# Kernel tuning notes

Hardware: AMD Instinct MI355X
Metric: run time of the kernel (lower is better)

The kernel has to match this reference:

```python
import jax, jax.numpy as jnp
import numpy as np

N_NODES = 50000
N_EDGES = 800000
X_DIM, EDGE_DIM, H_DIM, HOUT = 92, 80, 128, 128
N_CONV = 3
N_GRAPHS = 256
BN_EPS = 1e-5


def setup_inputs() -> dict:
    key = jax.random.key(0)
    ks = jax.random.split(key, 16)
    x = jax.random.normal(ks[0], (N_NODES, X_DIM), dtype=jnp.float32)
    edge_index = jax.random.randint(ks[1], (2, N_EDGES), 0, N_NODES, dtype=jnp.int64)
    edge_attr = jax.random.normal(ks[2], (N_EDGES, EDGE_DIM), dtype=jnp.float32)
    batch = jnp.sort(jax.random.randint(ks[3], (N_NODES,), 0, N_GRAPHS, dtype=jnp.int64))
    s = 0.05
    embed_W = jax.random.normal(ks[4], (X_DIM, H_DIM), dtype=jnp.float32) * s
    embed_b = jnp.zeros((H_DIM,), jnp.float32)
    in_dim = 2 * H_DIM + EDGE_DIM
    conv_W = jax.random.normal(ks[5], (N_CONV, in_dim, 2 * H_DIM), dtype=jnp.float32) * s
    conv_b = jnp.zeros((N_CONV, 2 * H_DIM), jnp.float32)
    bn_i_g = jnp.ones((N_CONV, 2 * H_DIM), jnp.float32)
    bn_i_b = jnp.zeros((N_CONV, 2 * H_DIM), jnp.float32)
    bn_o_g = jnp.ones((N_CONV, H_DIM), jnp.float32)
    bn_o_b = jnp.zeros((N_CONV, H_DIM), jnp.float32)
    lin_W = jax.random.normal(ks[6], (H_DIM, HOUT), dtype=jnp.float32) * s
    lin_b = jnp.zeros((HOUT,), jnp.float32)
    out_W = jax.random.normal(ks[7], (HOUT, 1), dtype=jnp.float32) * s
    out_b = jnp.zeros((1,), jnp.float32)
    return {"x": x, "edge_index": edge_index, "edge_attr": edge_attr, "batch": batch,
            "embed_W": embed_W, "embed_b": embed_b, "conv_W": conv_W, "conv_b": conv_b,
            "bn_i_g": bn_i_g, "bn_i_b": bn_i_b, "bn_o_g": bn_o_g, "bn_o_b": bn_o_b,
            "lin_W": lin_W, "lin_b": lin_b, "out_W": out_W, "out_b": out_b}


def _bn(h, gamma, beta):
    # training-mode BatchNorm1d: biased batch statistics
    mu = jnp.mean(h, axis=0)
    var = jnp.mean(jnp.square(h - mu), axis=0)
    return (h - mu) * jax.lax.rsqrt(var + BN_EPS) * gamma + beta


def _cgconv(x, edge_index, edge_attr, W, b, gi, bi, go, bo):
    src, dst = edge_index[0], edge_index[1]
    msg = jnp.concatenate([x[src], edge_attr, x[dst]], axis=1)  # [E, 2h+e]
    msg = msg @ W + b                                           # [E, 2h]
    msg = _bn(msg, gi, bi)
    filt, core = jnp.split(msg, 2, axis=1)
    gated = jax.nn.sigmoid(filt) * jax.nn.softplus(core)        # [E, h]
    agg = jax.ops.segment_sum(gated, src, num_segments=N_NODES)  # [N, h]
    agg = _bn(agg, go, bo)
    return jax.nn.softplus(x + agg)


def reference(x, edge_index, edge_attr, batch, embed_W, embed_b, conv_W, conv_b,
              bn_i_g, bn_i_b, bn_o_g, bn_o_b, lin_W, lin_b, out_W, out_b):
    h = x @ embed_W + embed_b  # [N, h_dim]
    for i in range(N_CONV):
        h = _cgconv(h, edge_index, edge_attr, conv_W[i], conv_b[i],
                    bn_i_g[i], bn_i_b[i], bn_o_g[i], bn_o_b[i])
    # mean pooling per graph
    sums = jax.ops.segment_sum(h, batch, num_segments=N_GRAPHS)
    cnts = jax.ops.segment_sum(jnp.ones((h.shape[0],), h.dtype), batch, num_segments=N_GRAPHS)
    pooled = sums / jnp.maximum(cnts, 1.0)[:, None]  # [G, h_dim]
    g = jax.nn.softplus(pooled @ lin_W + lin_b)
    return g @ out_W + out_b  # [G, 1]
```

## Files before the change

### kernel.cpp

```cpp
#include <hip/hip_runtime.h>

constexpr int NN = 50000;
constexpr int NE = 800000;
constexpr int XD = 92;
constexpr int ED = 80;
constexpr int HD = 128;
constexpr int C2 = 256;
constexpr int IND = 336;
constexpr int NC = 3;
constexpr int NG = 256;
constexpr int NTILES = NE / 64;
constexpr int WSZ_L = 16 * 3 * 64 * 8;
constexpr int WNP_L = 16 * 4 * 64 * 8;

#define DINL __device__ __forceinline__

typedef __attribute__((ext_vector_type(8))) short bf16x8;
typedef __attribute__((ext_vector_type(4))) float f32x4;

DINL short f2bf(float f) {
  unsigned u = __float_as_uint(f);
  u = (u + 0x7fffu + ((u >> 16) & 1u)) >> 16;
  return (short)u;
}
DINL float bf2f(unsigned short u) { return __uint_as_float(((unsigned)u) << 16); }
DINL float rcp_(float x) {
  float r;
  asm("v_rcp_f32 %0, %1" : "=v"(r) : "v"(x));
  return r;
}
DINL float softplusf_(float x) {
  return x > 20.f ? x : log1pf(__expf(x));
}
DINL float gate_(float f, float cr) {
  float e = __expf(-f);
  float s = rcp_(1.f + e);
  float t = __expf(cr);
  float l = (cr > 15.f) ? cr : __logf(1.f + t);
  return s * l;
}

template <int CTRL>
DINL int dpp_i(int old_, int src) {
  return __builtin_amdgcn_update_dpp(old_, src, CTRL, 0xF, 0xF, false);
}
template <int CTRL>
DINL float dpp_f(float old_, float src) {
  return __int_as_float(
      __builtin_amdgcn_update_dpp(__float_as_int(old_), __float_as_int(src), CTRL, 0xF, 0xF, false));
}
constexpr int SHR1 = 0x111, SHR2 = 0x112, SHR4 = 0x114, SHR8 = 0x118, SHL1 = 0x101;

__global__ __launch_bounds__(256) void k_embed(const float* __restrict__ x,
    const float* __restrict__ W, const float* __restrict__ b, float* __restrict__ h,
    unsigned short* __restrict__ hbf) {
  __shared__ float xs[2][XD];
  int t = threadIdx.x;
  int n0 = blockIdx.x * 2;
  for (int i = t; i < 2 * XD; i += 256) xs[i / XD][i % XD] = x[(size_t)n0 * XD + i];
  __syncthreads();
  int lo = t >> 7, c = t & 127;
  float acc = b[c];
  for (int k = 0; k < XD; ++k) acc = fmaf(xs[lo][k], W[k * HD + c], acc);
  h[(size_t)(n0 + lo) * HD + c] = acc;
  hbf[(size_t)(n0 + lo) * HD + c] = (unsigned short)f2bf(acc);
}

__global__ __launch_bounds__(256) void k_hist(const int* __restrict__ src,
                                              int* __restrict__ deg) {
  for (int e = blockIdx.x * 256 + threadIdx.x; e < NE; e += gridDim.x * 256)
    atomicAdd(&deg[src[e]], 1);
}

__global__ __launch_bounds__(1024) void k_scan(const int* __restrict__ deg,
                                               int* __restrict__ cursor) {
  __shared__ int sums[1024];
  int t = threadIdx.x;
  const int CH = 49;
  int b0 = t * CH;
  int s = 0;
  for (int i = 0; i < CH; ++i) {
    int idx = b0 + i;
    if (idx < NN) s += deg[idx];
  }
  sums[t] = s;
  __syncthreads();
  for (int off = 1; off < 1024; off <<= 1) {
    int v = (t >= off) ? sums[t - off] : 0;
    __syncthreads();
    sums[t] += v;
    __syncthreads();
  }
  int excl = (t == 0) ? 0 : sums[t - 1];
  for (int i = 0; i < CH; ++i) {
    int idx = b0 + i;
    if (idx < NN) {
      cursor[idx] = excl;
      excl += deg[idx];
    }
  }
}

__global__ __launch_bounds__(256) void k_scatter(const int* __restrict__ src,
    const int* __restrict__ dst, int* __restrict__ cursor, int* __restrict__ eid,
    int* __restrict__ ssort, int* __restrict__ dsort) {
  for (int e = blockIdx.x * 256 + threadIdx.x; e < NE; e += gridDim.x * 256) {
    int s = src[e];
    int pos = atomicAdd(&cursor[s], 1);
    eid[pos] = e;
    ssort[pos] = s;
    dsort[pos] = dst[e];
  }
}

__global__ __launch_bounds__(256) void k_wprep(const float* __restrict__ convW,
                                               unsigned short* __restrict__ Wswz) {
  int idx = blockIdx.x * 256 + threadIdx.x;
  if (idx >= NC * WSZ_L) return;
  int L = idx / WSZ_L;
  int rem = idx - L * WSZ_L;
  int mt = rem / 1536;
  int rem2 = rem - mt * 1536;
  int ks = rem2 >> 9;
  int lane = (rem2 >> 3) & 63;
  int j = rem2 & 7;
  int k = ks * 32 + (lane >> 4) * 8 + j;
  int m = mt * 16 + (lane & 15);
  float v = (k < ED) ? convW[(size_t)L * IND * C2 + (size_t)(HD + k) * C2 + m] : 0.f;
  Wswz[idx] = (unsigned short)f2bf(v);
}

__global__ __launch_bounds__(256) void k_wprep2(const float* __restrict__ convW,
                                                unsigned short* __restrict__ Wn) {
  int idx = blockIdx.x * 256 + threadIdx.x;
  if (idx >= NC * 2 * WNP_L) return;
  int Lh = idx >> 15;
  int L = Lh >> 1, half = Lh & 1;
  int rem = idx & 32767;
  int mt = rem >> 11;
  int rem2 = rem & 2047;
  int ks = rem2 >> 9;
  int lane = (rem2 >> 3) & 63;
  int j = rem2 & 7;
  int k = ks * 32 + (lane >> 4) * 8 + j;
  int m = mt * 16 + (lane & 15);
  int row = (half ? 208 : 0) + k;
  Wn[idx] = (unsigned short)f2bf(convW[(size_t)L * IND * C2 + (size_t)row * C2 + m]);
}

__global__ __launch_bounds__(256) void k_nodeproj2(const unsigned short* __restrict__ hbf,
    const unsigned short* __restrict__ Wn, int L,
    ushort4* __restrict__ P1, ushort4* __restrict__ P3) {
  __shared__ bf16x8 hls[1024];
  __shared__ ushort4 outls[4096];
  int t = threadIdx.x, w = t >> 6, l = t & 63, g = l >> 4, c = l & 15;
  int n0 = blockIdx.x * 64;
  int half = blockIdx.y;
  for (int i = t; i < 1024; i += 256) {
    int node = i >> 4, chunk = i & 15;
    int gn = n0 + node;
    if (gn >= NN) gn = NN - 1;
    bf16x8 v = *(const bf16x8*)(hbf + (size_t)gn * HD + chunk * 8);
    hls[node * 16 + (chunk ^ (node & 7))] = v;
  }
  __syncthreads();
  const bf16x8* Wf = (const bf16x8*)(Wn + ((size_t)(L * 2 + half)) * WNP_L);
  bf16x8 af[4][4];
#pragma unroll
  for (int mm = 0; mm < 4; ++mm)
#pragma unroll
    for (int ks = 0; ks < 4; ++ks) af[mm][ks] = Wf[((w * 4 + mm) * 4 + ks) * 64 + l];
  f32x4 acc[4][4];
#pragma unroll
  for (int mm = 0; mm < 4; ++mm)
#pragma unroll
    for (int nt = 0; nt < 4; ++nt)
#pragma unroll
      for (int i = 0; i < 4; ++i) acc[mm][nt][i] = 0.f;
#pragma unroll
  for (int nt = 0; nt < 4; ++nt) {
    int node = nt * 16 + c;
#pragma unroll
    for (int ks = 0; ks < 4; ++ks) {
      bf16x8 b = hls[node * 16 + ((4 * ks + g) ^ (node & 7))];
#pragma unroll
      for (int mm = 0; mm < 4; ++mm)
        acc[mm][nt] = __builtin_amdgcn_mfma_f32_16x16x32_bf16(af[mm][ks], b, acc[mm][nt], 0, 0, 0);
    }
  }
  __syncthreads();
#pragma unroll
  for (int mm = 0; mm < 4; ++mm)
#pragma unroll
    for (int nt = 0; nt < 4; ++nt) {
      int node = nt * 16 + c;
      int quad = (w * 4 + mm) * 4 + g;
      ushort4 st;
      st.x = (unsigned short)f2bf(acc[mm][nt][0]);
      st.y = (unsigned short)f2bf(acc[mm][nt][1]);
      st.z = (unsigned short)f2bf(acc[mm][nt][2]);
      st.w = (unsigned short)f2bf(acc[mm][nt][3]);
      outls[node * 64 + (quad ^ ((node & 7) << 3))] = st;
    }
  __syncthreads();
  ushort4* P = half ? P3 : P1;
  for (int i = t; i < 4096; i += 256) {
    int row = i >> 6, quad = i & 63;
    int gn = n0 + row;
    if (gn < NN) P[(size_t)gn * 64 + quad] = outls[row * 64 + (quad ^ ((row & 7) << 3))];
  }
}

__global__ __launch_bounds__(256) void k_eaprep(const int* __restrict__ eid,
    const float* __restrict__ ea, bf16x8* __restrict__ eaf) {
  int idx = blockIdx.x * 256 + threadIdx.x;
  if (idx >= NTILES * 768) return;
  int tile = idx / 768;
  int r = idx - tile * 768;
  int fr = r >> 6, l = r & 63;
  int nt = fr / 3, ks = fr - 3 * nt;
  int c = l & 15, g = l >> 4;
  int k0 = ks * 32 + g * 8;
  bf16x8 v;
  if (k0 < ED) {
    int e = eid[tile * 64 + nt * 16 + c];
    const float* p = ea + (size_t)e * ED + k0;
    float4 x0 = *(const float4*)p;
    float4 x1 = *(const float4*)(p + 4);
    v[0] = f2bf(x0.x); v[1] = f2bf(x0.y); v[2] = f2bf(x0.z); v[3] = f2bf(x0.w);
    v[4] = f2bf(x1.x); v[5] = f2bf(x1.y); v[6] = f2bf(x1.z); v[7] = f2bf(x1.w);
  } else {
#pragma unroll
    for (int j = 0; j < 8; ++j) v[j] = 0;
  }
  eaf[idx] = v;
}

__global__ __launch_bounds__(256) void k_estat2(
    const int* __restrict__ ssort, const int* __restrict__ dsort,
    const bf16x8* __restrict__ eaf, const unsigned short* __restrict__ Wswz,
    const float* __restrict__ bias, const ushort4* __restrict__ P1b,
    const ushort4* __restrict__ P3b, ushort4* __restrict__ msgc,
    float* __restrict__ stats) {
  int t = threadIdx.x;
  int w = t >> 6, l = t & 63;
  int g = l >> 4, c = l & 15;
  int mtg[4] = {2 * w, 2 * w + 1, 2 * w + 8, 2 * w + 9};
  const bf16x8* Wf = (const bf16x8*)Wswz;
  bf16x8 af[4][3];
  f32x4 bias4[4];
#pragma unroll
  for (int m = 0; m < 4; ++m) {
#pragma unroll
    for (int ks = 0; ks < 3; ++ks) af[m][ks] = Wf[(mtg[m] * 3 + ks) * 64 + l];
    float4 bb = ((const float4*)bias)[mtg[m] * 4 + g];
    bias4[m][0] = bb.x; bias4[m][1] = bb.y; bias4[m][2] = bb.z; bias4[m][3] = bb.w;
  }
  f32x4 ssum[4], ssq[4];
#pragma unroll
  for (int m = 0; m < 4; ++m)
#pragma unroll
    for (int i = 0; i < 4; ++i) { ssum[m][i] = 0.f; ssq[m][i] = 0.f; }

  for (int tile = blockIdx.x; tile < NTILES; tile += gridDim.x) {
    int e0 = tile * 64;
#pragma unroll
    for (int nt = 0; nt < 4; ++nt) {
      const bf16x8* bp = eaf + ((size_t)tile * 12 + nt * 3) * 64 + l;
      bf16x8 b0 = bp[0];
      bf16x8 b1 = bp[64];
      bf16x8 b2 = bp[128];
      f32x4 acc[4];
#pragma unroll
      for (int m = 0; m < 4; ++m) {
        acc[m][0] = 0.f; acc[m][1] = 0.f; acc[m][2] = 0.f; acc[m][3] = 0.f;
      }
#pragma unroll
      for (int m = 0; m < 4; ++m)
        acc[m] = __builtin_amdgcn_mfma_f32_16x16x32_bf16(af[m][0], b0, acc[m], 0, 0, 0);
#pragma unroll
      for (int m = 0; m < 4; ++m)
        acc[m] = __builtin_amdgcn_mfma_f32_16x16x32_bf16(af[m][1], b1, acc[m], 0, 0, 0);
#pragma unroll
      for (int m = 0; m < 4; ++m)
        acc[m] = __builtin_amdgcn_mfma_f32_16x16x32_bf16(af[m][2], b2, acc[m], 0, 0, 0);
      int s_ = ssort[e0 + nt * 16 + c];
      int d_ = dsort[e0 + nt * 16 + c];
#pragma unroll
      for (int m = 0; m < 4; ++m) {
        ushort4 q1 = P1b[(size_t)s_ * 64 + mtg[m] * 4 + g];
        ushort4 q3 = P3b[(size_t)d_ * 64 + mtg[m] * 4 + g];
        f32x4 ms;
        ms[0] = acc[m][0] + bias4[m][0] + bf2f(q1.x) + bf2f(q3.x);
        ms[1] = acc[m][1] + bias4[m][1] + bf2f(q1.y) + bf2f(q3.y);
        ms[2] = acc[m][2] + bias4[m][2] + bf2f(q1.z) + bf2f(q3.z);
        ms[3] = acc[m][3] + bias4[m][3] + bf2f(q1.w) + bf2f(q3.w);
#pragma unroll
        for (int i = 0; i < 4; ++i) {
          ssum[m][i] += ms[i];
          ssq[m][i] = fmaf(ms[i], ms[i], ssq[m][i]);
        }
        ushort4 st;
        st.x = (unsigned short)f2bf(ms[0]);
        st.y = (unsigned short)f2bf(ms[1]);
        st.z = (unsigned short)f2bf(ms[2]);
        st.w = (unsigned short)f2bf(ms[3]);
        msgc[(((size_t)tile * 4 + nt) * 16 + w * 4 + m) * 64 + l] = st;
      }
    }
  }
#pragma unroll
  for (int off = 1; off < 16; off <<= 1)
#pragma unroll
    for (int m = 0; m < 4; ++m)
#pragma unroll
      for (int i = 0; i < 4; ++i) {
        ssum[m][i] += __shfl_xor(ssum[m][i], off, 16);
        ssq[m][i] += __shfl_xor(ssq[m][i], off, 16);
      }
  if (c == 0) {
#pragma unroll
    for (int m = 0; m < 4; ++m)
#pragma unroll
      for (int i = 0; i < 4; ++i) {
        int ch = mtg[m] * 16 + 4 * g + i;
        atomicAdd(&stats[ch], ssum[m][i]);
        atomicAdd(&stats[C2 + ch], ssq[m][i]);
      }
  }
}

__global__ void k_bnfin(const float* __restrict__ stats, float invcount,
                        const float* __restrict__ gamma, const float* __restrict__ beta,
                        int nch, float* __restrict__ out) {
  int t = blockIdx.x * blockDim.x + threadIdx.x;
  if (t < nch) {
    float mean = stats[t] * invcount;
    float var = stats[nch + t] * invcount - mean * mean;
    float istd = rsqrtf(var + 1e-5f);
    float sc = gamma[t] * istd;
    out[t] = sc;
    out[nch + t] = beta[t] - mean * sc;
  }
}

__global__ __launch_bounds__(256) void k_apply2(
    const int* __restrict__ ssort, const ushort4* __restrict__ msgc,
    const float* __restrict__ bns, float* __restrict__ agg) {
  int t = threadIdx.x;
  int w = t >> 6, l = t & 63;
  int g = l >> 4, c = l & 15;
  int mtg[4] = {2 * w, 2 * w + 1, 2 * w + 8, 2 * w + 9};
  f32x4 sc4[4], sh4[4];
#pragma unroll
  for (int m = 0; m < 4; ++m) {
    float4 s1 = ((const float4*)bns)[mtg[m] * 4 + g];
    float4 s2 = ((const float4*)bns)[64 + mtg[m] * 4 + g];
    sc4[m][0] = s1.x; sc4[m][1] = s1.y; sc4[m][2] = s1.z; sc4[m][3] = s1.w;
    sh4[m][0] = s2.x; sh4[m][1] = s2.y; sh4[m][2] = s2.z; sh4[m][3] = s2.w;
  }
  for (int tile = blockIdx.x; tile < NTILES; tile += gridDim.x) {
    int e0 = tile * 64;
#pragma unroll
    for (int nt = 0; nt < 4; ++nt) {
      int s_ = ssort[e0 + nt * 16 + c];
      int ps = dpp_i<SHR1>(-1, s_);
      int hp = (ps != s_) ? c : 0;
      hp = max(hp, dpp_i<SHR1>(0, hp));
      hp = max(hp, dpp_i<SHR2>(0, hp));
      hp = max(hp, dpp_i<SHR4>(0, hp));
      hp = max(hp, dpp_i<SHR8>(0, hp));
      int ns = dpp_i<SHL1>(-1, s_);
      bool tail = (ns != s_);
      bool g1 = (c - 1) >= hp, g2 = (c - 2) >= hp, g4 = (c - 4) >= hp, g8 = (c - 8) >= hp;

      f32x4 v4[4];
#pragma unroll
      for (int m = 0; m < 4; ++m) {
        ushort4 mw = msgc[(((size_t)tile * 4 + nt) * 16 + w * 4 + m) * 64 + l];
        v4[m][0] = fmaf(bf2f(mw.x), sc4[m][0], sh4[m][0]);
        v4[m][1] = fmaf(bf2f(mw.y), sc4[m][1], sh4[m][1]);
        v4[m][2] = fmaf(bf2f(mw.z), sc4[m][2], sh4[m][2]);
        v4[m][3] = fmaf(bf2f(mw.w), sc4[m][3], sh4[m][3]);
      }
      float gg_[8];
#pragma unroll
      for (int p = 0; p < 2; ++p)
#pragma unroll
        for (int i = 0; i < 4; ++i)
          gg_[p * 4 + i] = gate_(v4[p][i], v4[p + 2][i]);
#pragma unroll
      for (int q = 0; q < 8; ++q) {
        float tv;
        tv = dpp_f<SHR1>(0.f, gg_[q]); gg_[q] += g1 ? tv : 0.f;
        tv = dpp_f<SHR2>(0.f, gg_[q]); gg_[q] += g2 ? tv : 0.f;
        tv = dpp_f<SHR4>(0.f, gg_[q]); gg_[q] += g4 ? tv : 0.f;
        tv = dpp_f<SHR8>(0.f, gg_[q]); gg_[q] += g8 ? tv : 0.f;
      }
      if (tail) {
#pragma unroll
        for (int p = 0; p < 2; ++p)
#pragma unroll
          for (int i = 0; i < 4; ++i)
            atomicAdd(&agg[(size_t)s_ * HD + mtg[p] * 16 + 4 * g + i], gg_[p * 4 + i]);
      }
    }
  }
}

__global__ __launch_bounds__(256) void k_aggstat(const float* __restrict__ agg,
                                                 float* __restrict__ stats) {
  int t = threadIdx.x;
  int c = t & 127, half = t >> 7;
  float s = 0.f, sq = 0.f;
  for (int n = blockIdx.x * 2 + half; n < NN; n += gridDim.x * 2) {
    float v = agg[(size_t)n * HD + c];
    s += v;
    sq = fmaf(v, v, sq);
  }
  __shared__ float shs[2][128], shq[2][128];
  shs[half][c] = s;
  shq[half][c] = sq;
  __syncthreads();
  if (t < 128) {
    atomicAdd(&stats[c], shs[0][c] + shs[1][c]);
    atomicAdd(&stats[128 + c], shq[0][c] + shq[1][c]);
  }
}

__global__ __launch_bounds__(256) void k_update(const float* __restrict__ h,
    const float* __restrict__ agg, const float* __restrict__ bns, float* __restrict__ hn,
    unsigned short* __restrict__ hbf) {
  int stride = gridDim.x * 256;
  for (int i = blockIdx.x * 256 + threadIdx.x; i < NN * HD; i += stride) {
    int c = i & 127;
    float v = h[i] + fmaf(agg[i], bns[c], bns[128 + c]);
    float r = softplusf_(v);
    hn[i] = r;
    hbf[i] = (unsigned short)f2bf(r);
  }
}

__global__ __launch_bounds__(256) void k_pool(const float* __restrict__ h,
    const int* __restrict__ batch, float* __restrict__ psum, int* __restrict__ pcnt) {
  int stride = gridDim.x * 256;
  for (int i = blockIdx.x * 256 + threadIdx.x; i < NN * HD; i += stride) {
    int n = i >> 7, c = i & 127;
    int g = batch[n];
    atomicAdd(&psum[g * HD + c], h[i]);
    if (c == 0) atomicAdd(&pcnt[g], 1);
  }
}

__global__ __launch_bounds__(128) void k_head(const float* __restrict__ psum,
    const int* __restrict__ pcnt, const float* __restrict__ linW,
    const float* __restrict__ linb, const float* __restrict__ outW,
    const float* __restrict__ outb, float* __restrict__ out) {
  __shared__ float pl[HD];
  __shared__ float red[2];
  int g = blockIdx.x, t = threadIdx.x;
  float cnt = fmaxf((float)pcnt[g], 1.f);
  pl[t] = psum[g * HD + t] / cnt;
  __syncthreads();
  float acc = linb[t];
  for (int k = 0; k < HD; ++k) acc = fmaf(pl[k], linW[k * HD + t], acc);
  float term = softplusf_(acc) * outW[t];
#pragma unroll
  for (int off = 32; off > 0; off >>= 1) term += __shfl_down(term, off, 64);
  if ((t & 63) == 0) red[t >> 6] = term;
  __syncthreads();
  if (t == 0) out[g] = red[0] + red[1] + outb[0];
}

extern "C" void kernel_launch(void* const* d_in, const int* in_sizes, int n_in,
                              void* d_out, int out_size, void* d_ws, size_t ws_size,
                              hipStream_t stream) {
  const float* x = (const float*)d_in[0];
  const int* ei = (const int*)d_in[1];
  const float* ea = (const float*)d_in[2];
  const int* batch = (const int*)d_in[3];
  const float* embW = (const float*)d_in[4];
  const float* embb = (const float*)d_in[5];
  const float* convW = (const float*)d_in[6];
  const float* convb = (const float*)d_in[7];
  const float* big = (const float*)d_in[8];
  const float* bib = (const float*)d_in[9];
  const float* bog = (const float*)d_in[10];
  const float* bob = (const float*)d_in[11];
  const float* linW = (const float*)d_in[12];
  const float* linb = (const float*)d_in[13];
  const float* outW = (const float*)d_in[14];
  const float* outb = (const float*)d_in[15];
  float* out = (float*)d_out;

  float* wsf = (float*)d_ws;
  size_t off = 0;
  auto alloc = [&](size_t n) {
    float* p = wsf + off;
    off += (n + 3) & ~(size_t)3;
    return p;
  };
  float* h0 = alloc((size_t)NN * HD);
  float* h1 = alloc((size_t)NN * HD);
  unsigned short* hbf = (unsigned short*)alloc((size_t)NN * HD / 2);
  ushort4* P1b = (ushort4*)alloc((size_t)NN * C2 / 2);
  ushort4* P3b = (ushort4*)alloc((size_t)NN * C2 / 2);
  float* agg = alloc((size_t)NN * HD);
  float* st_i = alloc(2 * C2);
  float* bnsi = alloc(2 * C2);
  float* st_o = alloc(2 * HD);
  float* bnso = alloc(2 * HD);
  float* psum = alloc((size_t)NG * HD);
  int* pcnt = (int*)alloc(NG);
  int* deg = (int*)alloc(NN);
  int* cursor = (int*)alloc(NN);
  int* eid = (int*)alloc(NE);
  int* ssort = (int*)alloc(NE);
  int* dsort = (int*)alloc(NE);
  unsigned short* Wswz = (unsigned short*)alloc((NC * WSZ_L + 1) / 2);
  unsigned short* Wn = (unsigned short*)alloc((NC * 2 * WNP_L + 1) / 2);
  bf16x8* eaf = (bf16x8*)alloc((size_t)NTILES * 768 * 4);
  ushort4* msgc = (ushort4*)alloc((size_t)NE * C2 / 2);

  const int* srcp = ei;
  const int* dstp = ei + NE;

  hipMemsetAsync(deg, 0, NN * sizeof(int), stream);
  k_hist<<<2048, 256, 0, stream>>>(srcp, deg);
  k_scan<<<1, 1024, 0, stream>>>(deg, cursor);
  k_scatter<<<2048, 256, 0, stream>>>(srcp, dstp, cursor, eid, ssort, dsort);

  k_wprep<<<(NC * WSZ_L + 255) / 256, 256, 0, stream>>>(convW, Wswz);
  k_wprep2<<<(NC * 2 * WNP_L + 255) / 256, 256, 0, stream>>>(convW, Wn);
  k_eaprep<<<(NTILES * 768 + 255) / 256, 256, 0, stream>>>(eid, ea, eaf);
  k_embed<<<NN / 2, 256, 0, stream>>>(x, embW, embb, h0, hbf);

  float* hc = h0;
  float* hn = h1;
  for (int L = 0; L < NC; ++L) {
    const unsigned short* Wl = Wswz + (size_t)L * WSZ_L;
    const float* bL = convb + (size_t)L * C2;
    hipMemsetAsync(st_i, 0, 2 * C2 * sizeof(float), stream);
    hipMemsetAsync(st_o, 0, 2 * HD * sizeof(float), stream);
    hipMemsetAsync(agg, 0, (size_t)NN * HD * sizeof(float), stream);

    dim3 npgrid((NN + 63) / 64, 2);
    k_nodeproj2<<<npgrid, 256, 0, stream>>>(hbf, Wn, L, P1b, P3b);
    k_estat2<<<2500, 256, 0, stream>>>(ssort, dsort, eaf, Wl, bL, P1b, P3b, msgc, st_i);
    k_bnfin<<<1, 256, 0, stream>>>(st_i, 1.f / NE, big + L * C2, bib + L * C2, C2, bnsi);
    k_apply2<<<2500, 256, 0, stream>>>(ssort, msgc, bnsi, agg);
    k_aggstat<<<512, 256, 0, stream>>>(agg, st_o);
    k_bnfin<<<1, 256, 0, stream>>>(st_o, 1.f / NN, bog + L * HD, bob + L * HD, HD, bnso);
    k_update<<<2048, 256, 0, stream>>>(hc, agg, bnso, hn, hbf);
    float* tmp = hc; hc = hn; hn = tmp;
  }

  hipMemsetAsync(psum, 0, (size_t)NG * HD * sizeof(float), stream);
  hipMemsetAsync(pcnt, 0, NG * sizeof(int), stream);
  k_pool<<<2048, 256, 0, stream>>>(hc, batch, psum, pcnt);
  k_head<<<NG, 128, 0, stream>>>(psum, pcnt, linW, linb, outW, outb, out);
}
```

Before: 2.669 ms.

## Prefetch edge indices and batch gathers in estat, fuse BN finalize into consumers

k_estat2 now loads all edge-attribute fragments and P1b/P3b gathers for a tile up front and prefetches the next tile's src/dst indices. It also drops the conv bias, which cancels under training-mode BatchNorm, and adds an occupancy hint. k_apply2 batches its message loads per tile. The separate k_bnfin launches are removed and the scale/shift are computed inline from raw stats in k_apply2 and k_update. This targets gather latency and small-kernel launch overhead, at the cost of more registers and repeated rsqrt per element in k_update.

```diff
diff --git a/kernel.cpp b/kernel.cpp
--- a/kernel.cpp
+++ b/kernel.cpp
@@ -29,9 +29,7 @@
   asm("v_rcp_f32 %0, %1" : "=v"(r) : "v"(x));
   return r;
 }
-DINL float softplusf_(float x) {
-  return x > 20.f ? x : log1pf(__expf(x));
-}
+DINL float softplusf_(float x) { return x > 20.f ? x : log1pf(__expf(x)); }
 DINL float gate_(float f, float cr) {
   float e = __expf(-f);
   float s = rcp_(1.f + e);
@@ -236,65 +234,82 @@
   eaf[idx] = v;
 }
 
-__global__ __launch_bounds__(256) void k_estat2(
+__global__ __launch_bounds__(256, 2) void k_estat2(
     const int* __restrict__ ssort, const int* __restrict__ dsort,
     const bf16x8* __restrict__ eaf, const unsigned short* __restrict__ Wswz,
-    const float* __restrict__ bias, const ushort4* __restrict__ P1b,
-    const ushort4* __restrict__ P3b, ushort4* __restrict__ msgc,
-    float* __restrict__ stats) {
+    const ushort4* __restrict__ P1b, const ushort4* __restrict__ P3b,
+    ushort4* __restrict__ msgc, float* __restrict__ stats) {
   int t = threadIdx.x;
   int w = t >> 6, l = t & 63;
   int g = l >> 4, c = l & 15;
   int mtg[4] = {2 * w, 2 * w + 1, 2 * w + 8, 2 * w + 9};
   const bf16x8* Wf = (const bf16x8*)Wswz;
   bf16x8 af[4][3];
-  f32x4 bias4[4];
-#pragma unroll
-  for (int m = 0; m < 4; ++m) {
+#pragma unroll
+  for (int m = 0; m < 4; ++m)
 #pragma unroll
     for (int ks = 0; ks < 3; ++ks) af[m][ks] = Wf[(mtg[m] * 3 + ks) * 64 + l];
-    float4 bb = ((const float4*)bias)[mtg[m] * 4 + g];
-    bias4[m][0] = bb.x; bias4[m][1] = bb.y; bias4[m][2] = bb.z; bias4[m][3] = bb.w;
-  }
   f32x4 ssum[4], ssq[4];
 #pragma unroll
   for (int m = 0; m < 4; ++m)
 #pragma unroll
     for (int i = 0; i < 4; ++i) { ssum[m][i] = 0.f; ssq[m][i] = 0.f; }
 
-  for (int tile = blockIdx.x; tile < NTILES; tile += gridDim.x) {
-    int e0 = tile * 64;
+  const int stride = gridDim.x;
+  int tile = blockIdx.x;
+  int s_[4], d_[4];
+  if (tile < NTILES) {
 #pragma unroll
     for (int nt = 0; nt < 4; ++nt) {
-      const bf16x8* bp = eaf + ((size_t)tile * 12 + nt * 3) * 64 + l;
-      bf16x8 b0 = bp[0];
-      bf16x8 b1 = bp[64];
-      bf16x8 b2 = bp[128];
+      s_[nt] = ssort[tile * 64 + nt * 16 + c];
+      d_[nt] = dsort[tile * 64 + nt * 16 + c];
+    }
+  }
+  for (; tile < NTILES; tile += stride) {
+    bf16x8 b_[12];
+    const bf16x8* bp = eaf + (size_t)tile * 768 + l;
+#pragma unroll
+    for (int fr = 0; fr < 12; ++fr) b_[fr] = bp[fr * 64];
+    ushort4 q1[4][4], q3[4][4];
+#pragma unroll
+    for (int nt = 0; nt < 4; ++nt)
+#pragma unroll
+      for (int m = 0; m < 4; ++m) {
+        q1[nt][m] = P1b[(size_t)s_[nt] * 64 + mtg[m] * 4 + g];
+        q3[nt][m] = P3b[(size_t)d_[nt] * 64 + mtg[m] * 4 + g];
+      }
+    int sn[4], dn[4];
+    int tn = tile + stride;
+    if (tn < NTILES) {
+#pragma unroll
+      for (int nt = 0; nt < 4; ++nt) {
+        sn[nt] = ssort[tn * 64 + nt * 16 + c];
+        dn[nt] = dsort[tn * 64 + nt * 16 + c];
+      }
+    } else {
+#pragma unroll
+      for (int nt = 0; nt < 4; ++nt) { sn[nt] = 0; dn[nt] = 0; }
+    }
+#pragma unroll
+    for (int nt = 0; nt < 4; ++nt) {
       f32x4 acc[4];
 #pragma unroll
       for (int m = 0; m < 4; ++m) {
         acc[m][0] = 0.f; acc[m][1] = 0.f; acc[m][2] = 0.f; acc[m][3] = 0.f;
       }
 #pragma unroll
-      for (int m = 0; m < 4; ++m)
-        acc[m] = __builtin_amdgcn_mfma_f32_16x16x32_bf16(af[m][0], b0, acc[m], 0, 0, 0);
-#pragma unroll
-      for (int m = 0; m < 4; ++m)
-        acc[m] = __builtin_amdgcn_mfma_f32_16x16x32_bf16(af[m][1], b1, acc[m], 0, 0, 0);
-#pragma unroll
-      for (int m = 0; m < 4; ++m)
-        acc[m] = __builtin_amdgcn_mfma_f32_16x16x32_bf16(af[m][2], b2, acc[m], 0, 0, 0);
-      int s_ = ssort[e0 + nt * 16 + c];
-      int d_ = dsort[e0 + nt * 16 + c];
+      for (int ks = 0; ks < 3; ++ks)
+#pragma unroll
+        for (int m = 0; m < 4; ++m)
+          acc[m] = __builtin_amdgcn_mfma_f32_16x16x32_bf16(af[m][ks], b_[nt * 3 + ks],
+                                                           acc[m], 0, 0, 0);
 #pragma unroll
       for (int m = 0; m < 4; ++m) {
-        ushort4 q1 = P1b[(size_t)s_ * 64 + mtg[m] * 4 + g];
-        ushort4 q3 = P3b[(size_t)d_ * 64 + mtg[m] * 4 + g];
         f32x4 ms;
-        ms[0] = acc[m][0] + bias4[m][0] + bf2f(q1.x) + bf2f(q3.x);
-        ms[1] = acc[m][1] + bias4[m][1] + bf2f(q1.y) + bf2f(q3.y);
-        ms[2] = acc[m][2] + bias4[m][2] + bf2f(q1.z) + bf2f(q3.z);
-        ms[3] = acc[m][3] + bias4[m][3] + bf2f(q1.w) + bf2f(q3.w);
+        ms[0] = acc[m][0] + bf2f(q1[nt][m].x) + bf2f(q3[nt][m].x);
+        ms[1] = acc[m][1] + bf2f(q1[nt][m].y) + bf2f(q3[nt][m].y);
+        ms[2] = acc[m][2] + bf2f(q1[nt][m].z) + bf2f(q3[nt][m].z);
+        ms[3] = acc[m][3] + bf2f(q1[nt][m].w) + bf2f(q3[nt][m].w);
 #pragma unroll
         for (int i = 0; i < 4; ++i) {
           ssum[m][i] += ms[i];
@@ -308,6 +323,8 @@
         msgc[(((size_t)tile * 4 + nt) * 16 + w * 4 + m) * 64 + l] = st;
       }
     }
+#pragma unroll
+    for (int nt = 0; nt < 4; ++nt) { s_[nt] = sn[nt]; d_[nt] = dn[nt]; }
   }
 #pragma unroll
   for (int off = 1; off < 16; off <<= 1)
@@ -330,58 +347,56 @@
   }
 }
 
-__global__ void k_bnfin(const float* __restrict__ stats, float invcount,
-                        const float* __restrict__ gamma, const float* __restrict__ beta,
-                        int nch, float* __restrict__ out) {
-  int t = blockIdx.x * blockDim.x + threadIdx.x;
-  if (t < nch) {
-    float mean = stats[t] * invcount;
-    float var = stats[nch + t] * invcount - mean * mean;
-    float istd = rsqrtf(var + 1e-5f);
-    float sc = gamma[t] * istd;
-    out[t] = sc;
-    out[nch + t] = beta[t] - mean * sc;
-  }
-}
-
 __global__ __launch_bounds__(256) void k_apply2(
     const int* __restrict__ ssort, const ushort4* __restrict__ msgc,
-    const float* __restrict__ bns, float* __restrict__ agg) {
+    const float* __restrict__ st, const float* __restrict__ gammaI,
+    const float* __restrict__ betaI, float* __restrict__ agg) {
   int t = threadIdx.x;
   int w = t >> 6, l = t & 63;
   int g = l >> 4, c = l & 15;
   int mtg[4] = {2 * w, 2 * w + 1, 2 * w + 8, 2 * w + 9};
   f32x4 sc4[4], sh4[4];
 #pragma unroll
-  for (int m = 0; m < 4; ++m) {
-    float4 s1 = ((const float4*)bns)[mtg[m] * 4 + g];
-    float4 s2 = ((const float4*)bns)[64 + mtg[m] * 4 + g];
-    sc4[m][0] = s1.x; sc4[m][1] = s1.y; sc4[m][2] = s1.z; sc4[m][3] = s1.w;
-    sh4[m][0] = s2.x; sh4[m][1] = s2.y; sh4[m][2] = s2.z; sh4[m][3] = s2.w;
-  }
+  for (int m = 0; m < 4; ++m)
+#pragma unroll
+    for (int i = 0; i < 4; ++i) {
+      int ch = mtg[m] * 16 + 4 * g + i;
+      float mean = st[ch] * (1.f / NE);
+      float var = st[C2 + ch] * (1.f / NE) - mean * mean;
+      float scv = gammaI[ch] * rsqrtf(var + 1e-5f);
+      sc4[m][i] = scv;
+      sh4[m][i] = betaI[ch] - mean * scv;
+    }
   for (int tile = blockIdx.x; tile < NTILES; tile += gridDim.x) {
     int e0 = tile * 64;
+    int s_[4];
+#pragma unroll
+    for (int nt = 0; nt < 4; ++nt) s_[nt] = ssort[e0 + nt * 16 + c];
+    ushort4 mw[4][4];
+#pragma unroll
+    for (int nt = 0; nt < 4; ++nt)
+#pragma unroll
+      for (int m = 0; m < 4; ++m)
+        mw[nt][m] = msgc[(((size_t)tile * 4 + nt) * 16 + w * 4 + m) * 64 + l];
 #pragma unroll
     for (int nt = 0; nt < 4; ++nt) {
-      int s_ = ssort[e0 + nt * 16 + c];
-      int ps = dpp_i<SHR1>(-1, s_);
-      int hp = (ps != s_) ? c : 0;
+      int sv = s_[nt];
+      int ps = dpp_i<SHR1>(-1, sv);
+      int hp = (ps != sv) ? c : 0;
       hp = max(hp, dpp_i<SHR1>(0, hp));
       hp = max(hp, dpp_i<SHR2>(0, hp));
       hp = max(hp, dpp_i<SHR4>(0, hp));
       hp = max(hp, dpp_i<SHR8>(0, hp));
-      int ns = dpp_i<SHL1>(-1, s_);
-      bool tail = (ns != s_);
+      int ns = dpp_i<SHL1>(-1, sv);
+      bool tail = (ns != sv);
       bool g1 = (c - 1) >= hp, g2 = (c - 2) >= hp, g4 = (c - 4) >= hp, g8 = (c - 8) >= hp;
-
       f32x4 v4[4];
 #pragma unroll
       for (int m = 0; m < 4; ++m) {
-        ushort4 mw = msgc[(((size_t)tile * 4 + nt) * 16 + w * 4 + m) * 64 + l];
-        v4[m][0] = fmaf(bf2f(mw.x), sc4[m][0], sh4[m][0]);
-        v4[m][1] = fmaf(bf2f(mw.y), sc4[m][1], sh4[m][1]);
-        v4[m][2] = fmaf(bf2f(mw.z), sc4[m][2], sh4[m][2]);
-        v4[m][3] = fmaf(bf2f(mw.w), sc4[m][3], sh4[m][3]);
+        v4[m][0] = fmaf(bf2f(mw[nt][m].x), sc4[m][0], sh4[m][0]);
+        v4[m][1] = fmaf(bf2f(mw[nt][m].y), sc4[m][1], sh4[m][1]);
+        v4[m][2] = fmaf(bf2f(mw[nt][m].z), sc4[m][2], sh4[m][2]);
+        v4[m][3] = fmaf(bf2f(mw[nt][m].w), sc4[m][3], sh4[m][3]);
       }
       float gg_[8];
 #pragma unroll
@@ -402,7 +417,7 @@
         for (int p = 0; p < 2; ++p)
 #pragma unroll
           for (int i = 0; i < 4; ++i)
-            atomicAdd(&agg[(size_t)s_ * HD + mtg[p] * 16 + 4 * g + i], gg_[p * 4 + i]);
+            atomicAdd(&agg[(size_t)sv * HD + mtg[p] * 16 + 4 * g + i], gg_[p * 4 + i]);
       }
     }
   }
@@ -429,12 +444,17 @@
 }
 
 __global__ __launch_bounds__(256) void k_update(const float* __restrict__ h,
-    const float* __restrict__ agg, const float* __restrict__ bns, float* __restrict__ hn,
-    unsigned short* __restrict__ hbf) {
+    const float* __restrict__ agg, const float* __restrict__ st_o,
+    const float* __restrict__ bog, const float* __restrict__ bob,
+    float* __restrict__ hn, unsigned short* __restrict__ hbf) {
   int stride = gridDim.x * 256;
   for (int i = blockIdx.x * 256 + threadIdx.x; i < NN * HD; i += stride) {
     int c = i & 127;
-    float v = h[i] + fmaf(agg[i], bns[c], bns[128 + c]);
+    float mean = st_o[c] * (1.f / NN);
+    float var = st_o[128 + c] * (1.f / NN) - mean * mean;
+    float scv = bog[c] * rsqrtf(var + 1e-5f);
+    float shv = bob[c] - mean * scv;
+    float v = h[i] + fmaf(agg[i], scv, shv);
     float r = softplusf_(v);
     hn[i] = r;
     hbf[i] = (unsigned short)f2bf(r);
@@ -482,7 +502,6 @@
   const float* embW = (const float*)d_in[4];
   const float* embb = (const float*)d_in[5];
   const float* convW = (const float*)d_in[6];
-  const float* convb = (const float*)d_in[7];
   const float* big = (const float*)d_in[8];
   const float* bib = (const float*)d_in[9];
   const float* bog = (const float*)d_in[10];
@@ -507,9 +526,7 @@
   ushort4* P3b = (ushort4*)alloc((size_t)NN * C2 / 2);
   float* agg = alloc((size_t)NN * HD);
   float* st_i = alloc(2 * C2);
-  float* bnsi = alloc(2 * C2);
   float* st_o = alloc(2 * HD);
-  float* bnso = alloc(2 * HD);
   float* psum = alloc((size_t)NG * HD);
   int* pcnt = (int*)alloc(NG);
   int* deg = (int*)alloc(NN);
@@ -539,19 +556,16 @@
   float* hn = h1;
   for (int L = 0; L < NC; ++L) {
     const unsigned short* Wl = Wswz + (size_t)L * WSZ_L;
-    const float* bL = convb + (size_t)L * C2;
     hipMemsetAsync(st_i, 0, 2 * C2 * sizeof(float), stream);
     hipMemsetAsync(st_o, 0, 2 * HD * sizeof(float), stream);
     hipMemsetAsync(agg, 0, (size_t)NN * HD * sizeof(float), stream);
 
     dim3 npgrid((NN + 63) / 64, 2);
     k_nodeproj2<<<npgrid, 256, 0, stream>>>(hbf, Wn, L, P1b, P3b);
-    k_estat2<<<2500, 256, 0, stream>>>(ssort, dsort, eaf, Wl, bL, P1b, P3b, msgc, st_i);
-    k_bnfin<<<1, 256, 0, stream>>>(st_i, 1.f / NE, big + L * C2, bib + L * C2, C2, bnsi);
-    k_apply2<<<2500, 256, 0, stream>>>(ssort, msgc, bnsi, agg);
+    k_estat2<<<2500, 256, 0, stream>>>(ssort, dsort, eaf, Wl, P1b, P3b, msgc, st_i);
+    k_apply2<<<2500, 256, 0, stream>>>(ssort, msgc, st_i, big + L * C2, bib + L * C2, agg);
     k_aggstat<<<512, 256, 0, stream>>>(agg, st_o);
-    k_bnfin<<<1, 256, 0, stream>>>(st_o, 1.f / NN, bog + L * HD, bob + L * HD, HD, bnso);
-    k_update<<<2048, 256, 0, stream>>>(hc, agg, bnso, hn, hbf);
+    k_update<<<2048, 256, 0, stream>>>(hc, agg, st_o, bog + L * HD, bob + L * HD, hn, hbf);
     float* tmp = hc; hc = hn; hn = tmp;
   }
 
```

Result: faster. 2.291 ms (-14.1%).
